# Optimization experiments

Measured on AMD Instinct MI355X. Metric: run time of the kernel, lower is better.

Reference implementation:

```python
import jax, jax.numpy as jnp
import numpy as np

HID = 64
N_NODES = 2048
BATCH = 8
SEQ = 32
AVG_DEG = 16


def _normalized_laplacian(rng, n, avg_deg):
    # symmetric 0/1 adjacency with ~avg_deg neighbors per node, zero diagonal
    p = avg_deg / n
    A = (rng.random((n, n)) < p).astype(np.float32)
    A = np.maximum(A, A.T)
    np.fill_diagonal(A, 0.0)
    d = A.sum(axis=1)
    dinv = np.where(d > 0, 1.0 / np.sqrt(np.maximum(d, 1e-12)), 0.0).astype(np.float32)
    L = -dinv[:, None] * A * dinv[None, :]
    L[np.arange(n), np.arange(n)] = np.where(d > 0, 1.0, 0.0)  # scipy laplacian(normed=True)
    return L


def setup_inputs() -> dict:
    key = jax.random.key(0)
    k1, k2, k3 = jax.random.split(key, 3)
    rng = np.random.default_rng(0)
    L = _normalized_laplacian(rng, N_NODES, AVG_DEG)
    scale_g = 1.0 / np.sqrt(HID + 1)
    return {
        "x": jax.random.normal(k1, (BATCH, SEQ, N_NODES), dtype=jnp.float32),
        "L_sym": jnp.asarray(L),
        "W_gates": jax.random.normal(k2, (2 * HID, HID + 1), dtype=jnp.float32) * scale_g,
        "b_gates": jnp.ones((2 * HID,), dtype=jnp.float32),
        "W_cand": jax.random.normal(k3, (HID, HID + 1), dtype=jnp.float32) * scale_g,
        "b_cand": jnp.ones((HID,), dtype=jnp.float32),
    }


def reference(x, L_sym, W_gates, b_gates, W_cand, b_cand):
    B, S, N = x.shape
    H = W_cand.shape[0]

    def cell(xt, state_flat, W, b):
        # xt: [B,N], state_flat: [B,N*H]
        s = state_flat.reshape(B, N, H)
        feats = jnp.concatenate([xt[..., None], s], axis=-1)          # [B,N,H+1]
        diff = jnp.einsum('mn,bnh->bmh', L_sym, feats)                # Laplacian diffusion
        out = jnp.einsum('bnh,oh->bno', diff, W) + b                  # [B,N,out]
        return out.reshape(B, -1)                                     # node-major flatten (matches torch)

    def step(state, xt):
        gates = jax.nn.sigmoid(cell(xt, state, W_gates, b_gates))     # [B, 2*N*H]
        half = N * H
        r, u = gates[:, :half], gates[:, half:]                       # flat split, as in torch .split
        cand = jnp.tanh(cell(xt, r * state, W_cand, b_cand))          # [B, N*H]
        new_h = u * state + (1.0 - u) * cand
        return new_h, new_h

    state0 = jnp.zeros((B, N * H), dtype=x.dtype)
    _, outs = jax.lax.scan(step, state0, jnp.transpose(x, (1, 0, 2)))  # [S,B,N*H]
    return outs
```

## Files before the change

### kernel.cpp

```cpp
#include <hip/hip_runtime.h>
#include <math.h>

#define N_NODES 2048
#define HID 64
#define BATCH 8
#define SEQ 32
#define CAP 64
#define TB 256
#define NH (N_NODES*HID)
#define WS2 72
#define CSA2 132
#define CSB2 68

typedef __attribute__((ext_vector_type(8))) _Float16 half8;
typedef __attribute__((ext_vector_type(2))) _Float16 half2f;
typedef __attribute__((ext_vector_type(8))) _Float16 f16x8;
typedef __attribute__((ext_vector_type(4))) float f32x4;

__device__ __forceinline__ float fast_sig(float s) {
  return 1.f / (1.f + __expf(-s));
}
__device__ __forceinline__ float fast_tanh(float s) {
  float e = __expf(-2.f * fabsf(s));
  float t = 1.f - 2.f * e / (1.f + e);
  return copysignf(t, s);
}

__global__ __launch_bounds__(256) void k_build_ell(
    const float* __restrict__ L, float* __restrict__ ell_val,
    _Float16* __restrict__ ell_valh, int* __restrict__ ell_colh,
    int* __restrict__ ell_cnt) {
  int wave = (blockIdx.x * blockDim.x + threadIdx.x) >> 6;
  int lane = threadIdx.x & 63;
  if (wave >= N_NODES) return;
  const float* row = L + (size_t)wave * N_NODES;
  int base = 0;
  for (int c = 0; c < N_NODES / 64; ++c) {
    int col = c * 64 + lane;
    float v = row[col];
    bool nz = (v != 0.0f);
    unsigned long long mask = __ballot(nz);
    int before = __popcll(mask & ((1ull << lane) - 1ull));
    if (nz) {
      int slot = base + before;
      if (slot < CAP) {
        ell_colh[wave * CAP + slot] = col * HID;
        ell_val[wave * CAP + slot] = v;
        ell_valh[wave * CAP + slot] = (_Float16)v;
      }
    }
    base += __popcll(mask);
  }
  if (base > CAP) base = CAP;
  int pad = (base + 7) & ~7;
  if (pad > CAP) pad = CAP;
  for (int s = base + lane; s < pad; s += 64) {
    ell_colh[wave * CAP + s] = 0;
    ell_val[wave * CAP + s] = 0.f;
    ell_valh[wave * CAP + s] = (_Float16)0.f;
  }
  if (lane == 0) ell_cnt[wave] = pad;
}

__global__ __launch_bounds__(256) void k_prep(
    const float* __restrict__ Wg, const float* __restrict__ Wc,
    _Float16* __restrict__ Wg16, _Float16* __restrict__ Wc16,
    float* __restrict__ wgx, float* __restrict__ wcx) {
  int tid = blockIdx.x * blockDim.x + threadIdx.x;
  int nthr = gridDim.x * blockDim.x;
  for (int i = tid; i < 128 * WS2; i += nthr) {
    int o = i / WS2, h = i % WS2;
    Wg16[i] = (h < 64) ? (_Float16)Wg[o * 65 + 1 + h] : (_Float16)0.f;
  }
  for (int i = tid; i < 64 * WS2; i += nthr) {
    int o = i / WS2, h = i % WS2;
    Wc16[i] = (h < 64) ? (_Float16)Wc[o * 65 + 1 + h] : (_Float16)0.f;
  }
  if (tid < 128) wgx[tid] = Wg[tid * 65];
  else if (tid < 192) wcx[tid - 128] = Wc[(tid - 128) * 65];
}

__global__ __launch_bounds__(256) void k_xt(const float* __restrict__ x,
                                            float* __restrict__ xT) {
  __shared__ float s[32][65];
  int n0  = (blockIdx.x & 63) * 32;
  int tb0 = (blockIdx.x >> 6) * 64;
  for (int idx = threadIdx.x; idx < 32 * 64; idx += 256) {
    int ln = idx & 31, ltb = idx >> 5;
    int tb = tb0 + ltb; int b = tb & 7, t = tb >> 3;
    s[ln][ltb] = x[((size_t)b * SEQ + t) * N_NODES + n0 + ln];
  }
  __syncthreads();
  for (int idx = threadIdx.x; idx < 32 * 64; idx += 256) {
    int ln = idx >> 6, ltb = idx & 63;
    xT[(size_t)(n0 + ln) * TB + tb0 + ltb] = s[ln][ltb];
  }
}

__global__ __launch_bounds__(512) void k_spmm_x(
    const float* __restrict__ xT, const float* __restrict__ ell_val,
    const int* __restrict__ ell_colh, const int* __restrict__ ell_cnt,
    float* __restrict__ LxT) {
  int m = (blockIdx.x * blockDim.x + threadIdx.x) >> 6;
  int lane = threadIdx.x & 63;
  if (m >= N_NODES) return;
  const int* cp = ell_colh + m * CAP;
  const float* vp = ell_val + m * CAP;
  int cnt = ell_cnt[m];
  float4 acc = {0.f, 0.f, 0.f, 0.f};
  for (int k = 0; k < cnt; k += 4) {
    int4 c = *(const int4*)(cp + k);
    float4 v = *(const float4*)(vp + k);
    float4 xa = *(const float4*)&xT[(size_t)c.x * 4 + lane * 4];
    float4 xb = *(const float4*)&xT[(size_t)c.y * 4 + lane * 4];
    float4 xc = *(const float4*)&xT[(size_t)c.z * 4 + lane * 4];
    float4 xd = *(const float4*)&xT[(size_t)c.w * 4 + lane * 4];
    acc.x = fmaf(v.x, xa.x, acc.x); acc.y = fmaf(v.x, xa.y, acc.y);
    acc.z = fmaf(v.x, xa.z, acc.z); acc.w = fmaf(v.x, xa.w, acc.w);
    acc.x = fmaf(v.y, xb.x, acc.x); acc.y = fmaf(v.y, xb.y, acc.y);
    acc.z = fmaf(v.y, xb.z, acc.z); acc.w = fmaf(v.y, xb.w, acc.w);
    acc.x = fmaf(v.z, xc.x, acc.x); acc.y = fmaf(v.z, xc.y, acc.y);
    acc.z = fmaf(v.z, xc.z, acc.z); acc.w = fmaf(v.z, xc.w, acc.w);
    acc.x = fmaf(v.w, xd.x, acc.x); acc.y = fmaf(v.w, xd.y, acc.y);
    acc.z = fmaf(v.w, xd.z, acc.z); acc.w = fmaf(v.w, xd.w, acc.w);
  }
  *(float4*)&LxT[(size_t)m * TB + lane * 4] = acc;
}

__global__ __launch_bounds__(256, 4) void k_gates(
    const half8* __restrict__ statepk, const float* __restrict__ LxT,
    const _Float16* __restrict__ ell_valh, const int* __restrict__ ell_colh,
    const int* __restrict__ ell_cnt, const _Float16* __restrict__ Wg16,
    const float* __restrict__ wgx, const float* __restrict__ bg,
    half8* __restrict__ rspk, half8* __restrict__ upk, int t) {
  __shared__ __align__(16) _Float16 sdiff[32 * WS2];
  __shared__ __align__(16) float sC[32 * CSA2];
  int wv = threadIdx.x >> 6, lane = threadIdx.x & 63;
  int m = blockIdx.x * 4 + wv;
  const half8* pk = statepk + lane;
  const int* cp = ell_colh + m * CAP;
  const _Float16* vp = ell_valh + m * CAP;
  int cnt = ell_cnt[m];
  int l15 = lane & 15, lq = lane >> 4;
  f16x8 afrag[2][2];
  {
    int ot0 = (wv * 4) >> 1;
    #pragma unroll
    for (int oo = 0; oo < 2; ++oo)
      #pragma unroll
      for (int s = 0; s < 2; ++s)
        afrag[oo][s] = *(const f16x8*)&Wg16[((ot0 + oo) * 16 + l15) * WS2 +
                                            s * 32 + lq * 8];
  }
  half2f a01 = {0, 0}, a23 = {0, 0}, a45 = {0, 0}, a67 = {0, 0};
  for (int k = 0; k < cnt; k += 8) {
    int4 ca = *(const int4*)(cp + k);
    int4 cb = *(const int4*)(cp + k + 4);
    half8 vv = *(const half8*)(vp + k);
#define GATH(C, V) { half8 hv = pk[C]; \
    const half2f* h2 = (const half2f*)&hv; \
    half2f vs = {V, V}; \
    a01 += vs * h2[0]; a23 += vs * h2[1]; \
    a45 += vs * h2[2]; a67 += vs * h2[3]; }
    GATH(ca.x, vv[0]) GATH(ca.y, vv[1]) GATH(ca.z, vv[2]) GATH(ca.w, vv[3])
    GATH(cb.x, vv[4]) GATH(cb.y, vv[5]) GATH(cb.z, vv[6]) GATH(cb.w, vv[7])
#undef GATH
  }
  {
    int r0 = wv * 8;
    sdiff[(r0 + 0) * WS2 + lane] = a01[0];
    sdiff[(r0 + 1) * WS2 + lane] = a01[1];
    sdiff[(r0 + 2) * WS2 + lane] = a23[0];
    sdiff[(r0 + 3) * WS2 + lane] = a23[1];
    sdiff[(r0 + 4) * WS2 + lane] = a45[0];
    sdiff[(r0 + 5) * WS2 + lane] = a45[1];
    sdiff[(r0 + 6) * WS2 + lane] = a67[0];
    sdiff[(r0 + 7) * WS2 + lane] = a67[1];
  }
  __syncthreads();
  #pragma unroll
  for (int tt = 0; tt < 4; ++tt) {
    int tid = wv * 4 + tt;
    int ot = tid >> 1, rt = tid & 1;
    f32x4 acc = {0.f, 0.f, 0.f, 0.f};
    #pragma unroll
    for (int s = 0; s < 2; ++s) {
      f16x8 bf = *(const f16x8*)&sdiff[(rt * 16 + l15) * WS2 + s * 32 + lq * 8];
      acc = __builtin_amdgcn_mfma_f32_16x16x32_f16(afrag[tt >> 1][s], bf, acc,
                                                   0, 0, 0);
    }
    int R = rt * 16 + l15;
    int O = ot * 16 + lq * 4;
    *(f32x4*)&sC[R * CSA2 + O] = acc;
  }
  __syncthreads();
  float4 LxLo = *(const float4*)&LxT[(size_t)m * TB + t * BATCH];
  float4 LxHi = *(const float4*)&LxT[(size_t)m * TB + t * BATCH + 4];
  float Lx8[8] = {LxLo.x, LxLo.y, LxLo.z, LxLo.w,
                  LxHi.x, LxHi.y, LxHi.z, LxHi.w};
  int o0 = lane, o1 = lane + 64;
  float wx0 = wgx[o0], bg0 = bg[o0];
  float wx1 = wgx[o1], bg1 = bg[o1];
  float s0[8], s1[8];
  #pragma unroll
  for (int b = 0; b < 8; ++b) {
    int R = wv * 8 + b;
    s0[b] = sC[R * CSA2 + o0] + fmaf(Lx8[b], wx0, bg0);
    s1[b] = sC[R * CSA2 + o1] + fmaf(Lx8[b], wx1, bg1);
  }
  if (m < N_NODES / 2) {
    half8 sp0 = pk[m * 128];
    half8 sp1 = pk[m * 128 + 64];
    half8 r0, r1;
    #pragma unroll
    for (int b = 0; b < 8; ++b) {
      r0[b] = (_Float16)(fast_sig(s0[b]) * (float)sp0[b]);
      r1[b] = (_Float16)(fast_sig(s1[b]) * (float)sp1[b]);
    }
    half8* rp = rspk + lane;
    rp[m * 128] = r0;
    rp[m * 128 + 64] = r1;
  } else {
    int mm = m - N_NODES / 2;
    half8 u0, u1;
    #pragma unroll
    for (int b = 0; b < 8; ++b) {
      u0[b] = (_Float16)fast_sig(s0[b]);
      u1[b] = (_Float16)fast_sig(s1[b]);
    }
    half8* up2 = upk + lane;
    up2[mm * 128] = u0;
    up2[mm * 128 + 64] = u1;
  }
}

__global__ __launch_bounds__(256, 4) void k_cand(
    const half8* __restrict__ statepk, const float* __restrict__ LxT,
    const _Float16* __restrict__ ell_valh, const int* __restrict__ ell_colh,
    const int* __restrict__ ell_cnt, const _Float16* __restrict__ Wc16,
    const float* __restrict__ wcx, const float* __restrict__ bc,
    const half8* __restrict__ rspk, const half8* __restrict__ upk,
    half8* __restrict__ statepk_next, float* __restrict__ out, int t) {
  __shared__ __align__(16) _Float16 sdiff[32 * WS2];
  __shared__ __align__(16) float sC[32 * CSB2];
  int wv = threadIdx.x >> 6, lane = threadIdx.x & 63;
  int m = blockIdx.x * 4 + wv;
  const half8* rk = rspk + lane;
  const int* cp = ell_colh + m * CAP;
  const _Float16* vp = ell_valh + m * CAP;
  int cnt = ell_cnt[m];
  int l15 = lane & 15, lq = lane >> 4;
  f16x8 afrag[2];
  #pragma unroll
  for (int s = 0; s < 2; ++s)
    afrag[s] = *(const f16x8*)&Wc16[(wv * 16 + l15) * WS2 + s * 32 + lq * 8];
  half2f a01 = {0, 0}, a23 = {0, 0}, a45 = {0, 0}, a67 = {0, 0};
  for (int k = 0; k < cnt; k += 8) {
    int4 ca = *(const int4*)(cp + k);
    int4 cb = *(const int4*)(cp + k + 4);
    half8 vv = *(const half8*)(vp + k);
#define GATH(C, V) { half8 hv = rk[C]; \
    const half2f* h2 = (const half2f*)&hv; \
    half2f vs = {V, V}; \
    a01 += vs * h2[0]; a23 += vs * h2[1]; \
    a45 += vs * h2[2]; a67 += vs * h2[3]; }
    GATH(ca.x, vv[0]) GATH(ca.y, vv[1]) GATH(ca.z, vv[2]) GATH(ca.w, vv[3])
    GATH(cb.x, vv[4]) GATH(cb.y, vv[5]) GATH(cb.z, vv[6]) GATH(cb.w, vv[7])
#undef GATH
  }
  {
    int r0 = wv * 8;
    sdiff[(r0 + 0) * WS2 + lane] = a01[0];
    sdiff[(r0 + 1) * WS2 + lane] = a01[1];
    sdiff[(r0 + 2) * WS2 + lane] = a23[0];
    sdiff[(r0 + 3) * WS2 + lane] = a23[1];
    sdiff[(r0 + 4) * WS2 + lane] = a45[0];
    sdiff[(r0 + 5) * WS2 + lane] = a45[1];
    sdiff[(r0 + 6) * WS2 + lane] = a67[0];
    sdiff[(r0 + 7) * WS2 + lane] = a67[1];
  }
  __syncthreads();
  #pragma unroll
  for (int tt = 0; tt < 2; ++tt) {
    int rt = tt;
    f32x4 acc = {0.f, 0.f, 0.f, 0.f};
    #pragma unroll
    for (int s = 0; s < 2; ++s) {
      f16x8 bf = *(const f16x8*)&sdiff[(rt * 16 + l15) * WS2 + s * 32 + lq * 8];
      acc = __builtin_amdgcn_mfma_f32_16x16x32_f16(afrag[s], bf, acc, 0, 0, 0);
    }
    int R = rt * 16 + l15;
    int O = wv * 16 + lq * 4;
    *(f32x4*)&sC[R * CSB2 + O] = acc;
  }
  __syncthreads();
  float4 LxLo = *(const float4*)&LxT[(size_t)m * TB + t * BATCH];
  float4 LxHi = *(const float4*)&LxT[(size_t)m * TB + t * BATCH + 4];
  float Lx8[8] = {LxLo.x, LxLo.y, LxLo.z, LxLo.w,
                  LxHi.x, LxHi.y, LxHi.z, LxHi.w};
  float wxc = wcx[lane], bbc = bc[lane];
  float s[8];
  #pragma unroll
  for (int b = 0; b < 8; ++b) {
    int R = wv * 8 + b;
    s[b] = sC[R * CSB2 + lane] + fmaf(Lx8[b], wxc, bbc);
  }
  half8 hp = (statepk + lane)[m * 64];
  half8 uu = (upk + lane)[m * 64];
  half8 np;
  float* op = out + (size_t)t * BATCH * NH + m * HID + lane;
  #pragma unroll
  for (int b = 0; b < 8; ++b) {
    float u = (float)uu[b];
    float nh = u * (float)hp[b] + (1.f - u) * fast_tanh(s[b]);
    np[b] = (_Float16)nh;
    op[(size_t)b * NH] = nh;
  }
  (statepk_next + lane)[m * 64] = np;
}

extern "C" void kernel_launch(void* const* d_in, const int* in_sizes, int n_in,
                              void* d_out, int out_size, void* d_ws, size_t ws_size,
                              hipStream_t stream) {
  const float* x  = (const float*)d_in[0];
  const float* L  = (const float*)d_in[1];
  const float* Wg = (const float*)d_in[2];
  const float* bg = (const float*)d_in[3];
  const float* Wc = (const float*)d_in[4];
  const float* bc = (const float*)d_in[5];
  float* out = (float*)d_out;
  float* ws = (float*)d_ws;

  float*    ell_val  = ws;
  int*      ell_colh = (int*)(ws + (size_t)N_NODES * CAP);
  _Float16* ell_valh = (_Float16*)(ws + (size_t)2 * N_NODES * CAP);
  int*      ell_cnt  = (int*)(ws + (size_t)2 * N_NODES * CAP + N_NODES * CAP / 2);
  float* xT  = ws + (size_t)2 * N_NODES * CAP + N_NODES * CAP / 2 + N_NODES;
  float* LxT = xT + (size_t)N_NODES * TB;
  float* fend = LxT + (size_t)N_NODES * TB;
  half8* stA  = (half8*)fend;
  half8* stB  = stA + (size_t)N_NODES * HID;
  half8* rspk = stB + (size_t)N_NODES * HID;
  half8* upk  = rspk + (size_t)N_NODES * HID;
  _Float16* Wg16 = (_Float16*)(upk + (size_t)N_NODES * HID);
  _Float16* Wc16 = Wg16 + 128 * WS2;
  float* wgx = (float*)(Wc16 + 64 * WS2);
  float* wcx = wgx + 128;

  k_build_ell<<<N_NODES / 4, 256, 0, stream>>>(L, ell_val, ell_valh, ell_colh,
                                               ell_cnt);
  k_prep<<<64, 256, 0, stream>>>(Wg, Wc, Wg16, Wc16, wgx, wcx);
  k_xt<<<256, 256, 0, stream>>>(x, xT);
  k_spmm_x<<<N_NODES / 8, 512, 0, stream>>>(xT, ell_val, ell_colh, ell_cnt, LxT);
  hipMemsetAsync(stA, 0, (size_t)N_NODES * HID * sizeof(half8), stream);

  half8* cur = stA;
  half8* nxt = stB;
  for (int t = 0; t < SEQ; ++t) {
    k_gates<<<N_NODES / 4, 256, 0, stream>>>(cur, LxT, ell_valh, ell_colh,
                                             ell_cnt, Wg16, wgx, bg, rspk, upk,
                                             t);
    k_cand<<<N_NODES / 4, 256, 0, stream>>>(cur, LxT, ell_valh, ell_colh,
                                            ell_cnt, Wc16, wcx, bc, rspk, upk,
                                            nxt, out, t);
    half8* tmp = cur; cur = nxt; nxt = tmp;
  }
}
```

Before: 650.9 us.

## Sort rows by nnz and process two matched rows per single-wave block

Adds a one-wave counting sort that orders rows by padded nonzero count. The gate and candidate kernels now run one 64-thread block per pair of similar-length rows, interleaving the two rows' gathers and doing all MFMA output tiles inside one wave without __syncthreads. ELL padding is zero-filled to CAP so the shorter row can safely run to the longer row's count. This targets load imbalance between waves of different degree and block-level sync. It doubles the block count and reloads weight fragments from global memory on every block.

```diff
diff --git a/kernel.cpp b/kernel.cpp
--- a/kernel.cpp
+++ b/kernel.cpp
@@ -52,14 +52,41 @@
     base += __popcll(mask);
   }
   if (base > CAP) base = CAP;
-  int pad = (base + 7) & ~7;
-  if (pad > CAP) pad = CAP;
-  for (int s = base + lane; s < pad; s += 64) {
+  for (int s = base + lane; s < CAP; s += 64) {
     ell_colh[wave * CAP + s] = 0;
     ell_val[wave * CAP + s] = 0.f;
     ell_valh[wave * CAP + s] = (_Float16)0.f;
   }
+  int pad = (base + 7) & ~7;
+  if (pad > CAP) pad = CAP;
   if (lane == 0) ell_cnt[wave] = pad;
+}
+
+__global__ __launch_bounds__(64) void k_sort(const int* __restrict__ ell_cnt,
+                                             int* __restrict__ rowmap) {
+  int lane = threadIdx.x;
+  int h[9];
+  #pragma unroll
+  for (int j = 0; j < 9; ++j) h[j] = 0;
+  for (int c = 0; c < N_NODES / 64; ++c) {
+    int v = ell_cnt[c * 64 + lane] >> 3;
+    #pragma unroll
+    for (int j = 0; j < 9; ++j) h[j] += __popcll(__ballot(v == j));
+  }
+  int cur[9];
+  int run = 0;
+  #pragma unroll
+  for (int j = 0; j < 9; ++j) { cur[j] = run; run += h[j]; }
+  for (int c = 0; c < N_NODES / 64; ++c) {
+    int v = ell_cnt[c * 64 + lane] >> 3;
+    #pragma unroll
+    for (int j = 0; j < 9; ++j) {
+      unsigned long long mask = __ballot(v == j);
+      int before = __popcll(mask & ((1ull << lane) - 1ull));
+      if (v == j) rowmap[cur[j] + before] = c * 64 + lane;
+      cur[j] += __popcll(mask);
+    }
+  }
 }
 
 __global__ __launch_bounds__(256) void k_prep(
@@ -127,196 +154,202 @@
   *(float4*)&LxT[(size_t)m * TB + lane * 4] = acc;
 }
 
-__global__ __launch_bounds__(256, 4) void k_gates(
+__global__ __launch_bounds__(64) void k_gates(
     const half8* __restrict__ statepk, const float* __restrict__ LxT,
     const _Float16* __restrict__ ell_valh, const int* __restrict__ ell_colh,
     const int* __restrict__ ell_cnt, const _Float16* __restrict__ Wg16,
     const float* __restrict__ wgx, const float* __restrict__ bg,
-    half8* __restrict__ rspk, half8* __restrict__ upk, int t) {
-  __shared__ __align__(16) _Float16 sdiff[32 * WS2];
-  __shared__ __align__(16) float sC[32 * CSA2];
-  int wv = threadIdx.x >> 6, lane = threadIdx.x & 63;
-  int m = blockIdx.x * 4 + wv;
+    half8* __restrict__ rspk, half8* __restrict__ upk,
+    const int* __restrict__ rowmap, int t) {
+  __shared__ __align__(16) _Float16 sdiff[16 * WS2];
+  __shared__ __align__(16) float sC[16 * CSA2];
+  int lane = threadIdx.x;
+  int mA = rowmap[blockIdx.x * 2];
+  int mB = rowmap[blockIdx.x * 2 + 1];
   const half8* pk = statepk + lane;
-  const int* cp = ell_colh + m * CAP;
-  const _Float16* vp = ell_valh + m * CAP;
-  int cnt = ell_cnt[m];
+  const int* cpA = ell_colh + mA * CAP;
+  const _Float16* vpA = ell_valh + mA * CAP;
+  const int* cpB = ell_colh + mB * CAP;
+  const _Float16* vpB = ell_valh + mB * CAP;
+  int cA = ell_cnt[mA], cB = ell_cnt[mB];
+  int cnt = (cA > cB) ? cA : cB;
+  half2f aA01={0,0},aA23={0,0},aA45={0,0},aA67={0,0};
+  half2f aB01={0,0},aB23={0,0},aB45={0,0},aB67={0,0};
+  for (int k = 0; k < cnt; k += 8) {
+    int4 caA = *(const int4*)(cpA + k);
+    int4 cbA = *(const int4*)(cpA + k + 4);
+    half8 vvA = *(const half8*)(vpA + k);
+    int4 caB = *(const int4*)(cpB + k);
+    int4 cbB = *(const int4*)(cpB + k + 4);
+    half8 vvB = *(const half8*)(vpB + k);
+#define GA(C, V) { half8 hv = pk[C]; const half2f* h2 = (const half2f*)&hv; \
+    half2f vs = {V, V}; aA01 += vs*h2[0]; aA23 += vs*h2[1]; \
+    aA45 += vs*h2[2]; aA67 += vs*h2[3]; }
+#define GB(C, V) { half8 hv = pk[C]; const half2f* h2 = (const half2f*)&hv; \
+    half2f vs = {V, V}; aB01 += vs*h2[0]; aB23 += vs*h2[1]; \
+    aB45 += vs*h2[2]; aB67 += vs*h2[3]; }
+    GA(caA.x, vvA[0]) GB(caB.x, vvB[0]) GA(caA.y, vvA[1]) GB(caB.y, vvB[1])
+    GA(caA.z, vvA[2]) GB(caB.z, vvB[2]) GA(caA.w, vvA[3]) GB(caB.w, vvB[3])
+    GA(cbA.x, vvA[4]) GB(cbB.x, vvB[4]) GA(cbA.y, vvA[5]) GB(cbB.y, vvB[5])
+    GA(cbA.z, vvA[6]) GB(cbB.z, vvB[6]) GA(cbA.w, vvA[7]) GB(cbB.w, vvB[7])
+#undef GA
+#undef GB
+  }
+  sdiff[ 0*WS2+lane]=aA01[0]; sdiff[ 1*WS2+lane]=aA01[1];
+  sdiff[ 2*WS2+lane]=aA23[0]; sdiff[ 3*WS2+lane]=aA23[1];
+  sdiff[ 4*WS2+lane]=aA45[0]; sdiff[ 5*WS2+lane]=aA45[1];
+  sdiff[ 6*WS2+lane]=aA67[0]; sdiff[ 7*WS2+lane]=aA67[1];
+  sdiff[ 8*WS2+lane]=aB01[0]; sdiff[ 9*WS2+lane]=aB01[1];
+  sdiff[10*WS2+lane]=aB23[0]; sdiff[11*WS2+lane]=aB23[1];
+  sdiff[12*WS2+lane]=aB45[0]; sdiff[13*WS2+lane]=aB45[1];
+  sdiff[14*WS2+lane]=aB67[0]; sdiff[15*WS2+lane]=aB67[1];
   int l15 = lane & 15, lq = lane >> 4;
-  f16x8 afrag[2][2];
-  {
-    int ot0 = (wv * 4) >> 1;
-    #pragma unroll
-    for (int oo = 0; oo < 2; ++oo)
-      #pragma unroll
-      for (int s = 0; s < 2; ++s)
-        afrag[oo][s] = *(const f16x8*)&Wg16[((ot0 + oo) * 16 + l15) * WS2 +
-                                            s * 32 + lq * 8];
-  }
-  half2f a01 = {0, 0}, a23 = {0, 0}, a45 = {0, 0}, a67 = {0, 0};
-  for (int k = 0; k < cnt; k += 8) {
-    int4 ca = *(const int4*)(cp + k);
-    int4 cb = *(const int4*)(cp + k + 4);
-    half8 vv = *(const half8*)(vp + k);
-#define GATH(C, V) { half8 hv = pk[C]; \
-    const half2f* h2 = (const half2f*)&hv; \
-    half2f vs = {V, V}; \
-    a01 += vs * h2[0]; a23 += vs * h2[1]; \
-    a45 += vs * h2[2]; a67 += vs * h2[3]; }
-    GATH(ca.x, vv[0]) GATH(ca.y, vv[1]) GATH(ca.z, vv[2]) GATH(ca.w, vv[3])
-    GATH(cb.x, vv[4]) GATH(cb.y, vv[5]) GATH(cb.z, vv[6]) GATH(cb.w, vv[7])
-#undef GATH
-  }
-  {
-    int r0 = wv * 8;
-    sdiff[(r0 + 0) * WS2 + lane] = a01[0];
-    sdiff[(r0 + 1) * WS2 + lane] = a01[1];
-    sdiff[(r0 + 2) * WS2 + lane] = a23[0];
-    sdiff[(r0 + 3) * WS2 + lane] = a23[1];
-    sdiff[(r0 + 4) * WS2 + lane] = a45[0];
-    sdiff[(r0 + 5) * WS2 + lane] = a45[1];
-    sdiff[(r0 + 6) * WS2 + lane] = a67[0];
-    sdiff[(r0 + 7) * WS2 + lane] = a67[1];
-  }
-  __syncthreads();
-  #pragma unroll
-  for (int tt = 0; tt < 4; ++tt) {
-    int tid = wv * 4 + tt;
-    int ot = tid >> 1, rt = tid & 1;
+  f16x8 bf0 = *(const f16x8*)&sdiff[l15 * WS2 + 0 * 32 + lq * 8];
+  f16x8 bf1 = *(const f16x8*)&sdiff[l15 * WS2 + 1 * 32 + lq * 8];
+  #pragma unroll
+  for (int ot = 0; ot < 8; ++ot) {
     f32x4 acc = {0.f, 0.f, 0.f, 0.f};
-    #pragma unroll
-    for (int s = 0; s < 2; ++s) {
-      f16x8 bf = *(const f16x8*)&sdiff[(rt * 16 + l15) * WS2 + s * 32 + lq * 8];
-      acc = __builtin_amdgcn_mfma_f32_16x16x32_f16(afrag[tt >> 1][s], bf, acc,
-                                                   0, 0, 0);
-    }
-    int R = rt * 16 + l15;
-    int O = ot * 16 + lq * 4;
-    *(f32x4*)&sC[R * CSA2 + O] = acc;
-  }
-  __syncthreads();
-  float4 LxLo = *(const float4*)&LxT[(size_t)m * TB + t * BATCH];
-  float4 LxHi = *(const float4*)&LxT[(size_t)m * TB + t * BATCH + 4];
-  float Lx8[8] = {LxLo.x, LxLo.y, LxLo.z, LxLo.w,
-                  LxHi.x, LxHi.y, LxHi.z, LxHi.w};
+    f16x8 af0 = *(const f16x8*)&Wg16[(ot * 16 + l15) * WS2 + 0 * 32 + lq * 8];
+    f16x8 af1 = *(const f16x8*)&Wg16[(ot * 16 + l15) * WS2 + 1 * 32 + lq * 8];
+    acc = __builtin_amdgcn_mfma_f32_16x16x32_f16(af0, bf0, acc, 0, 0, 0);
+    acc = __builtin_amdgcn_mfma_f32_16x16x32_f16(af1, bf1, acc, 0, 0, 0);
+    *(f32x4*)&sC[l15 * CSA2 + ot * 16 + lq * 4] = acc;
+  }
   int o0 = lane, o1 = lane + 64;
   float wx0 = wgx[o0], bg0 = bg[o0];
   float wx1 = wgx[o1], bg1 = bg[o1];
-  float s0[8], s1[8];
-  #pragma unroll
-  for (int b = 0; b < 8; ++b) {
-    int R = wv * 8 + b;
-    s0[b] = sC[R * CSA2 + o0] + fmaf(Lx8[b], wx0, bg0);
-    s1[b] = sC[R * CSA2 + o1] + fmaf(Lx8[b], wx1, bg1);
-  }
-  if (m < N_NODES / 2) {
-    half8 sp0 = pk[m * 128];
-    half8 sp1 = pk[m * 128 + 64];
-    half8 r0, r1;
+  int mm[2] = {mA, mB};
+  #pragma unroll
+  for (int nn = 0; nn < 2; ++nn) {
+    int m = mm[nn];
+    float4 LxLo = *(const float4*)&LxT[(size_t)m * TB + t * BATCH];
+    float4 LxHi = *(const float4*)&LxT[(size_t)m * TB + t * BATCH + 4];
+    float Lx8[8] = {LxLo.x, LxLo.y, LxLo.z, LxLo.w,
+                    LxHi.x, LxHi.y, LxHi.z, LxHi.w};
+    float s0[8], s1[8];
     #pragma unroll
     for (int b = 0; b < 8; ++b) {
-      r0[b] = (_Float16)(fast_sig(s0[b]) * (float)sp0[b]);
-      r1[b] = (_Float16)(fast_sig(s1[b]) * (float)sp1[b]);
-    }
-    half8* rp = rspk + lane;
-    rp[m * 128] = r0;
-    rp[m * 128 + 64] = r1;
-  } else {
-    int mm = m - N_NODES / 2;
-    half8 u0, u1;
-    #pragma unroll
-    for (int b = 0; b < 8; ++b) {
-      u0[b] = (_Float16)fast_sig(s0[b]);
-      u1[b] = (_Float16)fast_sig(s1[b]);
-    }
-    half8* up2 = upk + lane;
-    up2[mm * 128] = u0;
-    up2[mm * 128 + 64] = u1;
-  }
-}
-
-__global__ __launch_bounds__(256, 4) void k_cand(
+      int R = nn * 8 + b;
+      s0[b] = sC[R * CSA2 + o0] + fmaf(Lx8[b], wx0, bg0);
+      s1[b] = sC[R * CSA2 + o1] + fmaf(Lx8[b], wx1, bg1);
+    }
+    if (m < N_NODES / 2) {
+      half8 sp0 = pk[m * 128];
+      half8 sp1 = pk[m * 128 + 64];
+      half8 r0, r1;
+      #pragma unroll
+      for (int b = 0; b < 8; ++b) {
+        r0[b] = (_Float16)(fast_sig(s0[b]) * (float)sp0[b]);
+        r1[b] = (_Float16)(fast_sig(s1[b]) * (float)sp1[b]);
+      }
+      half8* rp = rspk + lane;
+      rp[m * 128] = r0;
+      rp[m * 128 + 64] = r1;
+    } else {
+      int mq = m - N_NODES / 2;
+      half8 u0, u1;
+      #pragma unroll
+      for (int b = 0; b < 8; ++b) {
+        u0[b] = (_Float16)fast_sig(s0[b]);
+        u1[b] = (_Float16)fast_sig(s1[b]);
+      }
+      half8* up2 = upk + lane;
+      up2[mq * 128] = u0;
+      up2[mq * 128 + 64] = u1;
+    }
+  }
+}
+
+__global__ __launch_bounds__(64) void k_cand(
     const half8* __restrict__ statepk, const float* __restrict__ LxT,
     const _Float16* __restrict__ ell_valh, const int* __restrict__ ell_colh,
     const int* __restrict__ ell_cnt, const _Float16* __restrict__ Wc16,
     const float* __restrict__ wcx, const float* __restrict__ bc,
     const half8* __restrict__ rspk, const half8* __restrict__ upk,
-    half8* __restrict__ statepk_next, float* __restrict__ out, int t) {
-  __shared__ __align__(16) _Float16 sdiff[32 * WS2];
-  __shared__ __align__(16) float sC[32 * CSB2];
-  int wv = threadIdx.x >> 6, lane = threadIdx.x & 63;
-  int m = blockIdx.x * 4 + wv;
+    half8* __restrict__ statepk_next, float* __restrict__ out,
+    const int* __restrict__ rowmap, int t) {
+  __shared__ __align__(16) _Float16 sdiff[16 * WS2];
+  __shared__ __align__(16) float sC[16 * CSB2];
+  int lane = threadIdx.x;
+  int mA = rowmap[blockIdx.x * 2];
+  int mB = rowmap[blockIdx.x * 2 + 1];
   const half8* rk = rspk + lane;
-  const int* cp = ell_colh + m * CAP;
-  const _Float16* vp = ell_valh + m * CAP;
-  int cnt = ell_cnt[m];
+  const int* cpA = ell_colh + mA * CAP;
+  const _Float16* vpA = ell_valh + mA * CAP;
+  const int* cpB = ell_colh + mB * CAP;
+  const _Float16* vpB = ell_valh + mB * CAP;
+  int cA = ell_cnt[mA], cB = ell_cnt[mB];
+  int cnt = (cA > cB) ? cA : cB;
+  half2f aA01={0,0},aA23={0,0},aA45={0,0},aA67={0,0};
+  half2f aB01={0,0},aB23={0,0},aB45={0,0},aB67={0,0};
+  for (int k = 0; k < cnt; k += 8) {
+    int4 caA = *(const int4*)(cpA + k);
+    int4 cbA = *(const int4*)(cpA + k + 4);
+    half8 vvA = *(const half8*)(vpA + k);
+    int4 caB = *(const int4*)(cpB + k);
+    int4 cbB = *(const int4*)(cpB + k + 4);
+    half8 vvB = *(const half8*)(vpB + k);
+#define GA(C, V) { half8 hv = rk[C]; const half2f* h2 = (const half2f*)&hv; \
+    half2f vs = {V, V}; aA01 += vs*h2[0]; aA23 += vs*h2[1]; \
+    aA45 += vs*h2[2]; aA67 += vs*h2[3]; }
+#define GB(C, V) { half8 hv = rk[C]; const half2f* h2 = (const half2f*)&hv; \
+    half2f vs = {V, V}; aB01 += vs*h2[0]; aB23 += vs*h2[1]; \
+    aB45 += vs*h2[2]; aB67 += vs*h2[3]; }
+    GA(caA.x, vvA[0]) GB(caB.x, vvB[0]) GA(caA.y, vvA[1]) GB(caB.y, vvB[1])
+    GA(caA.z, vvA[2]) GB(caB.z, vvB[2]) GA(caA.w, vvA[3]) GB(caB.w, vvB[3])
+    GA(cbA.x, vvA[4]) GB(cbB.x, vvB[4]) GA(cbA.y, vvA[5]) GB(cbB.y, vvB[5])
+    GA(cbA.z, vvA[6]) GB(cbB.z, vvB[6]) GA(cbA.w, vvA[7]) GB(cbB.w, vvB[7])
+#undef GA
+#undef GB
+  }
+  sdiff[ 0*WS2+lane]=aA01[0]; sdiff[ 1*WS2+lane]=aA01[1];
+  sdiff[ 2*WS2+lane]=aA23[0]; sdiff[ 3*WS2+lane]=aA23[1];
+  sdiff[ 4*WS2+lane]=aA45[0]; sdiff[ 5*WS2+lane]=aA45[1];
+  sdiff[ 6*WS2+lane]=aA67[0]; sdiff[ 7*WS2+lane]=aA67[1];
+  sdiff[ 8*WS2+lane]=aB01[0]; sdiff[ 9*WS2+lane]=aB01[1];
+  sdiff[10*WS2+lane]=aB23[0]; sdiff[11*WS2+lane]=aB23[1];
+  sdiff[12*WS2+lane]=aB45[0]; sdiff[13*WS2+lane]=aB45[1];
+  sdiff[14*WS2+lane]=aB67[0]; sdiff[15*WS2+lane]=aB67[1];
   int l15 = lane & 15, lq = lane >> 4;
-  f16x8 afrag[2];
-  #pragma unroll
-  for (int s = 0; s < 2; ++s)
-    afrag[s] = *(const f16x8*)&Wc16[(wv * 16 + l15) * WS2 + s * 32 + lq * 8];
-  half2f a01 = {0, 0}, a23 = {0, 0}, a45 = {0, 0}, a67 = {0, 0};
-  for (int k = 0; k < cnt; k += 8) {
-    int4 ca = *(const int4*)(cp + k);
-    int4 cb = *(const int4*)(cp + k + 4);
-    half8 vv = *(const half8*)(vp + k);
-#define GATH(C, V) { half8 hv = rk[C]; \
-    const half2f* h2 = (const half2f*)&hv; \
-    half2f vs = {V, V}; \
-    a01 += vs * h2[0]; a23 += vs * h2[1]; \
-    a45 += vs * h2[2]; a67 += vs * h2[3]; }
-    GATH(ca.x, vv[0]) GATH(ca.y, vv[1]) GATH(ca.z, vv[2]) GATH(ca.w, vv[3])
-    GATH(cb.x, vv[4]) GATH(cb.y, vv[5]) GATH(cb.z, vv[6]) GATH(cb.w, vv[7])
-#undef GATH
-  }
-  {
-    int r0 = wv * 8;
-    sdiff[(r0 + 0) * WS2 + lane] = a01[0];
-    sdiff[(r0 + 1) * WS2 + lane] = a01[1];
-    sdiff[(r0 + 2) * WS2 + lane] = a23[0];
-    sdiff[(r0 + 3) * WS2 + lane] = a23[1];
-    sdiff[(r0 + 4) * WS2 + lane] = a45[0];
-    sdiff[(r0 + 5) * WS2 + lane] = a45[1];
-    sdiff[(r0 + 6) * WS2 + lane] = a67[0];
-    sdiff[(r0 + 7) * WS2 + lane] = a67[1];
-  }
-  __syncthreads();
-  #pragma unroll
-  for (int tt = 0; tt < 2; ++tt) {
-    int rt = tt;
+  f16x8 bf0 = *(const f16x8*)&sdiff[l15 * WS2 + 0 * 32 + lq * 8];
+  f16x8 bf1 = *(const f16x8*)&sdiff[l15 * WS2 + 1 * 32 + lq * 8];
+  #pragma unroll
+  for (int ot = 0; ot < 4; ++ot) {
     f32x4 acc = {0.f, 0.f, 0.f, 0.f};
+    f16x8 af0 = *(const f16x8*)&Wc16[(ot * 16 + l15) * WS2 + 0 * 32 + lq * 8];
+    f16x8 af1 = *(const f16x8*)&Wc16[(ot * 16 + l15) * WS2 + 1 * 32 + lq * 8];
+    acc = __builtin_amdgcn_mfma_f32_16x16x32_f16(af0, bf0, acc, 0, 0, 0);
+    acc = __builtin_amdgcn_mfma_f32_16x16x32_f16(af1, bf1, acc, 0, 0, 0);
+    *(f32x4*)&sC[l15 * CSB2 + ot * 16 + lq * 4] = acc;
+  }
+  float wxc = wcx[lane], bbc = bc[lane];
+  int mm[2] = {mA, mB};
+  #pragma unroll
+  for (int nn = 0; nn < 2; ++nn) {
+    int m = mm[nn];
+    float4 LxLo = *(const float4*)&LxT[(size_t)m * TB + t * BATCH];
+    float4 LxHi = *(const float4*)&LxT[(size_t)m * TB + t * BATCH + 4];
+    float Lx8[8] = {LxLo.x, LxLo.y, LxLo.z, LxLo.w,
+                    LxHi.x, LxHi.y, LxHi.z, LxHi.w};
+    float s[8];
     #pragma unroll
-    for (int s = 0; s < 2; ++s) {
-      f16x8 bf = *(const f16x8*)&sdiff[(rt * 16 + l15) * WS2 + s * 32 + lq * 8];
-      acc = __builtin_amdgcn_mfma_f32_16x16x32_f16(afrag[s], bf, acc, 0, 0, 0);
-    }
-    int R = rt * 16 + l15;
-    int O = wv * 16 + lq * 4;
-    *(f32x4*)&sC[R * CSB2 + O] = acc;
-  }
-  __syncthreads();
-  float4 LxLo = *(const float4*)&LxT[(size_t)m * TB + t * BATCH];
-  float4 LxHi = *(const float4*)&LxT[(size_t)m * TB + t * BATCH + 4];
-  float Lx8[8] = {LxLo.x, LxLo.y, LxLo.z, LxLo.w,
-                  LxHi.x, LxHi.y, LxHi.z, LxHi.w};
-  float wxc = wcx[lane], bbc = bc[lane];
-  float s[8];
-  #pragma unroll
-  for (int b = 0; b < 8; ++b) {
-    int R = wv * 8 + b;
-    s[b] = sC[R * CSB2 + lane] + fmaf(Lx8[b], wxc, bbc);
-  }
-  half8 hp = (statepk + lane)[m * 64];
-  half8 uu = (upk + lane)[m * 64];
-  half8 np;
-  float* op = out + (size_t)t * BATCH * NH + m * HID + lane;
-  #pragma unroll
-  for (int b = 0; b < 8; ++b) {
-    float u = (float)uu[b];
-    float nh = u * (float)hp[b] + (1.f - u) * fast_tanh(s[b]);
-    np[b] = (_Float16)nh;
-    op[(size_t)b * NH] = nh;
-  }
-  (statepk_next + lane)[m * 64] = np;
+    for (int b = 0; b < 8; ++b) {
+      int R = nn * 8 + b;
+      s[b] = sC[R * CSB2 + lane] + fmaf(Lx8[b], wxc, bbc);
+    }
+    half8 hp = (statepk + lane)[m * 64];
+    half8 uu = (upk + lane)[m * 64];
+    half8 np;
+    float* op = out + (size_t)t * BATCH * NH + m * HID + lane;
+    #pragma unroll
+    for (int b = 0; b < 8; ++b) {
+      float u = (float)uu[b];
+      float nh = u * (float)hp[b] + (1.f - u) * fast_tanh(s[b]);
+      np[b] = (_Float16)nh;
+      op[(size_t)b * NH] = nh;
+    }
+    (statepk_next + lane)[m * 64] = np;
+  }
 }
 
 extern "C" void kernel_launch(void* const* d_in, const int* in_sizes, int n_in,
@@ -346,9 +379,11 @@
   _Float16* Wc16 = Wg16 + 128 * WS2;
   float* wgx = (float*)(Wc16 + 64 * WS2);
   float* wcx = wgx + 128;
+  int* rowmap = (int*)(wcx + 64);
 
   k_build_ell<<<N_NODES / 4, 256, 0, stream>>>(L, ell_val, ell_valh, ell_colh,
                                                ell_cnt);
+  k_sort<<<1, 64, 0, stream>>>(ell_cnt, rowmap);
   k_prep<<<64, 256, 0, stream>>>(Wg, Wc, Wg16, Wc16, wgx, wcx);
   k_xt<<<256, 256, 0, stream>>>(x, xT);
   k_spmm_x<<<N_NODES / 8, 512, 0, stream>>>(xT, ell_val, ell_colh, ell_cnt, LxT);
@@ -357,12 +392,12 @@
   half8* cur = stA;
   half8* nxt = stB;
   for (int t = 0; t < SEQ; ++t) {
-    k_gates<<<N_NODES / 4, 256, 0, stream>>>(cur, LxT, ell_valh, ell_colh,
-                                             ell_cnt, Wg16, wgx, bg, rspk, upk,
-                                             t);
-    k_cand<<<N_NODES / 4, 256, 0, stream>>>(cur, LxT, ell_valh, ell_colh,
-                                            ell_cnt, Wc16, wcx, bc, rspk, upk,
-                                            nxt, out, t);
+    k_gates<<<N_NODES / 2, 64, 0, stream>>>(cur, LxT, ell_valh, ell_colh,
+                                            ell_cnt, Wg16, wgx, bg, rspk, upk,
+                                            rowmap, t);
+    k_cand<<<N_NODES / 2, 64, 0, stream>>>(cur, LxT, ell_valh, ell_colh,
+                                           ell_cnt, Wc16, wcx, bc, rspk, upk,
+                                           nxt, out, rowmap, t);
     half8* tmp = cur; cur = nxt; nxt = tmp;
   }
 }
```

Result: slower. 673.1 us (+3.4%).
